# Kernel optimization log

Hardware: AMD Instinct MI355X
Metric: run time of the kernel (lower is better)

## Reference

```python
import jax, jax.numpy as jnp
import numpy as np

EPS = 1e-10      # normalizer eps from the torch module
IN_EPS = 1e-5    # torch InstanceNorm2d default eps
STRIDE = 2
PAD = 1


def _dw_conv_transpose(x, W):
    """Depthwise ConvTranspose2d applied for every output channel at once.

    x: [B, Cin, H, W]
    W: [Cin, Cout, kh, kw]  (W[:, i] is sub_convs[i].weight of shape [Cin, 1, kh, kw])
    returns: [B, Cin, Cout, H', W'] where channel (c, i) = convT of x[:, c] with W[c, i].
    """
    Cin, Cout, kh, kw = W.shape
    # Transposed conv == dilated conv with spatially flipped kernel,
    # lhs_dilation = stride, padding = k - 1 - pad (output_padding = 0).
    rhs = jnp.flip(W, axis=(-2, -1)).reshape(Cin * Cout, 1, kh, kw)
    pad_h = (kh - 1 - PAD, kh - 1 - PAD)
    pad_w = (kw - 1 - PAD, kw - 1 - PAD)
    out = jax.lax.conv_general_dilated(
        x, rhs,
        window_strides=(1, 1),
        padding=(pad_h, pad_w),
        lhs_dilation=(STRIDE, STRIDE),
        dimension_numbers=('NCHW', 'OIHW', 'NCHW'),
        feature_group_count=Cin,
    )  # [B, Cin*Cout, H', W'], group-major: group c -> channels c*Cout:(c+1)*Cout
    B = x.shape[0]
    return out.reshape(B, Cin, Cout, out.shape[2], out.shape[3])


def setup_inputs() -> dict:
    key = jax.random.key(0)
    k1, k2, k3 = jax.random.split(key, 3)
    B, Cin, Cout, H, Wd, K = 2, 64, 64, 48, 48, 4
    x = jax.random.normal(k1, (B, Cin, H, Wd), dtype=jnp.float32)
    # Positive-leaning weights keep the normalizer (convT of ones) away from zero.
    W = 0.05 + 0.1 * jax.random.uniform(k2, (Cin, Cout, K, K), dtype=jnp.float32)
    bias = 0.02 * jax.random.normal(k3, (Cout,), dtype=jnp.float32)
    return {"x": x, "W": W, "bias": bias}


def reference(x, W, bias):
    # numerator: depthwise convT of the input for every (in_ch, out_ch) pair
    num = _dw_conv_transpose(x, W)                       # [B, Cin, Cout, H', W']
    # normalizer: same convT applied to ones (batch-independent -> batch of 1)
    den = _dw_conv_transpose(jnp.ones_like(x[:1]), W) + EPS  # [1, Cin, Cout, H', W']
    out = jnp.sum(num / den, axis=1) + bias[None, :, None, None]  # [B, Cout, H', W']
    # InstanceNorm2d (no affine, biased variance) over spatial dims per (b, c)
    mean = jnp.mean(out, axis=(2, 3), keepdims=True)
    var = jnp.var(out, axis=(2, 3), keepdims=True)
    return (out - mean) / jnp.sqrt(var + IN_EPS)
```

## Files before the change

kernel.cpp:

```cpp
#include <hip/hip_runtime.h>

#define BB    2
#define CIN   64
#define NI    64
#define HIN   48
#define WIN   48
#define HO    96
#define WO    96
#define EPSN  1e-10f
#define IN_EPS 1e-5f
#define IMG   (HO*WO)
#define NIMG  (BB*NI)
#define PH    50
#define PW    52
#define XPN   (BB*CIN*PH*PW)

__global__ __launch_bounds__(256) void pad_kernel(const float* __restrict__ x,
                                                  float* __restrict__ xpad) {
    const int slice = blockIdx.x >> 1, half = blockIdx.x & 1;
    const float* xs = x + (size_t)slice * (HIN * WIN);
    float* xd = xpad + (size_t)slice * (PH * PW) + half * 25 * PW;
    for (int e = threadIdx.x; e < 25 * PW; e += 256) {
        const int rp = e / PW, pc = e - rp * PW;
        const int h = half * 25 + rp - 1, w = pc - 1;
        float v = 0.f;
        if ((unsigned)h < HIN && (unsigned)w < WIN) v = xs[h * WIN + w];
        xd[e] = v;
    }
}

template <int CS>
__global__ __launch_bounds__(256) void conv_kernel(
        const float* __restrict__ xpad, const float* __restrict__ Wt,
        float* __restrict__ part) {
    constexpr int NC = CIN / CS;
    const int bi = blockIdx.x, s = blockIdx.y;
    const int b = bi >> 6, i = bi & 63, c0 = s * NC;
    const int tid = threadIdx.x;
    const int ty = tid >> 4, tx = tid & 15;

    __shared__ __align__(16) float sF[NC * 16];
    __shared__ float sW[NC * 16];
    __shared__ float sR[NC * 16];
    __shared__ float sFix[384];

    for (int e = tid; e < NC * 16; e += 256) {
        const int c = e >> 4, j = e & 15;
        const float* wp = Wt + ((size_t)(c0 + c) * NI + i) * 16;
        sW[e] = wp[j];
        const int py = (j >> 3) & 1, px = (j >> 2) & 1, a = (j >> 1) & 1, bb = j & 1;
        const int kh = py ? (a ? 2 : 0) : (a ? 3 : 1);
        const int kw = px ? (bb ? 2 : 0) : (bb ? 3 : 1);
        const int r0 = py ? 0 : 1, r1 = py ? 2 : 3;
        const int q0 = px ? 0 : 1, q1 = px ? 2 : 3;
        const float den = wp[r0 * 4 + q0] + wp[r0 * 4 + q1]
                        + wp[r1 * 4 + q0] + wp[r1 * 4 + q1];
        sF[e] = wp[kh * 4 + kw] / (den + EPSN);
        const int cy = j >> 2, cx = j & 3;
        const int THn[4] = {1, 2, 2, 1};
        const int THv[4][2] = {{1, 1}, {0, 2}, {1, 3}, {2, 2}};
        float den2 = 0.f;
        for (int aa = 0; aa < THn[cy]; ++aa)
            for (int bb2 = 0; bb2 < THn[cx]; ++bb2)
                den2 += wp[THv[cy][aa] * 4 + THv[cx][bb2]];
        sR[e] = 1.f / (den2 + EPSN);
    }
    __syncthreads();

    float acc[6][6];
#pragma unroll
    for (int r = 0; r < 6; ++r)
#pragma unroll
        for (int j = 0; j < 6; ++j) acc[r][j] = 0.f;

    const float* xb = xpad + ((size_t)b * CIN + c0) * (PH * PW) + (3 * ty) * PW + 3 * tx;

#pragma unroll 2
    for (int c = 0; c < NC; ++c) {
        float g[16];
        const float4* gf = (const float4*)&sF[c * 16];
#pragma unroll
        for (int q = 0; q < 4; ++q) {
            const float4 t = gf[q];
            g[4 * q] = t.x; g[4 * q + 1] = t.y; g[4 * q + 2] = t.z; g[4 * q + 3] = t.w;
        }

        const float* xc = xb + c * (PH * PW);
        float xv[5][5];
#pragma unroll
        for (int rr = 0; rr < 5; ++rr)
#pragma unroll
            for (int cc = 0; cc < 5; ++cc) xv[rr][cc] = xc[rr * PW + cc];

#pragma unroll
        for (int r = 0; r < 6; ++r) {
            const int rhi = (r + 3) >> 1, rlo = rhi - 1, py = r & 1;
#pragma unroll
            for (int j = 0; j < 6; ++j) {
                const int chi = (j + 3) >> 1, clo = chi - 1, px = j & 1;
                const float* gg = &g[py * 8 + px * 4];
                acc[r][j] += xv[rhi][chi] * gg[0] + xv[rhi][clo] * gg[1]
                           + xv[rlo][chi] * gg[2] + xv[rlo][clo] * gg[3];
            }
        }
    }

    const float* xb2 = xpad + ((size_t)b * CIN + c0) * (PH * PW);
    for (int p = tid; p < 380; p += 256) {
        int y, xo;
        if (p < 96)       { y = 0;            xo = p; }
        else if (p < 192) { y = 95;           xo = p - 96; }
        else if (p < 286) { y = p - 192 + 1;  xo = 0; }
        else              { y = p - 286 + 1;  xo = 95; }
        const int hA = (y + 1) >> 1, hB = hA - 1;
        const int khA = (y & 1) ? 0 : 1, khB = khA + 2;
        const int wA = (xo + 1) >> 1, wB = wA - 1;
        const int kwA = (xo & 1) ? 0 : 1, kwB = kwA + 2;
        const int cy = (y == 0) ? 0 : (y == 95) ? 3 : ((y & 1) ? 1 : 2);
        const int cx = (xo == 0) ? 0 : (xo == 95) ? 3 : ((xo & 1) ? 1 : 2);
        const int cls = cy * 4 + cx;
        const int rA = (hA + 1) * PW, rB = (hB + 1) * PW;
        float v = 0.f;
        for (int c = 0; c < NC; ++c) {
            const float* xc = xb2 + c * (PH * PW);
            const float* wc = &sW[c * 16];
            const float num = xc[rA + wA + 1] * wc[khA * 4 + kwA]
                            + xc[rA + wB + 1] * wc[khA * 4 + kwB]
                            + xc[rB + wA + 1] * wc[khB * 4 + kwA]
                            + xc[rB + wB + 1] * wc[khB * 4 + kwB];
            v += num * sR[c * 16 + cls];
        }
        sFix[p] = v;
    }
    __syncthreads();

#pragma unroll
    for (int r = 0; r < 6; ++r)
#pragma unroll
        for (int j = 0; j < 6; ++j) {
            const int y = 6 * ty + r, xo = 6 * tx + j;
            if (y == 0)        acc[r][j] = sFix[xo];
            else if (y == 95)  acc[r][j] = sFix[96 + xo];
            else if (xo == 0)  acc[r][j] = sFix[192 + y - 1];
            else if (xo == 95) acc[r][j] = sFix[286 + y - 1];
        }

    float* pp = part + ((size_t)s * NIMG + bi) * IMG + (6 * ty) * WO + 6 * tx;
#pragma unroll
    for (int r = 0; r < 6; ++r)
#pragma unroll
        for (int jj = 0; jj < 3; ++jj) {
            float2 v;
            v.x = acc[r][2 * jj];
            v.y = acc[r][2 * jj + 1];
            *(float2*)(pp + r * WO + 2 * jj) = v;
        }
}

template <int CS>
__global__ __launch_bounds__(768) void epilogue_kernel(
        const float* __restrict__ part, const float* __restrict__ bias,
        float* __restrict__ out) {
    const int bi = blockIdx.x;
    const int tid = threadIdx.x;
    const float bv = bias[bi & 63];
    const float4* pb = (const float4*)part + (size_t)bi * (IMG / 4);
    const size_t stride4 = (size_t)NIMG * (IMG / 4);

    float4 v[3];
    float s1 = 0.f, s2 = 0.f;
#pragma unroll
    for (int k = 0; k < 3; ++k) {
        const int idx = k * 768 + tid;
        float4 t = pb[idx];
#pragma unroll
        for (int s = 1; s < CS; ++s) {
            const float4 q = pb[s * stride4 + idx];
            t.x += q.x; t.y += q.y; t.z += q.z; t.w += q.w;
        }
        t.x += bv; t.y += bv; t.z += bv; t.w += bv;
        v[k] = t;
        s1 += t.x + t.y + t.z + t.w;
        s2 += t.x * t.x + t.y * t.y + t.z * t.z + t.w * t.w;
    }

    __shared__ float red[24];
    __shared__ float stat[2];
#pragma unroll
    for (int off = 32; off > 0; off >>= 1) {
        s1 += __shfl_down(s1, off, 64);
        s2 += __shfl_down(s2, off, 64);
    }
    const int w = tid >> 6;
    if ((tid & 63) == 0) { red[w] = s1; red[12 + w] = s2; }
    __syncthreads();
    if (tid == 0) {
        float t1 = 0.f, t2 = 0.f;
#pragma unroll
        for (int k = 0; k < 12; ++k) { t1 += red[k]; t2 += red[12 + k]; }
        const float mean = t1 * (1.f / 9216.f);
        const float m2 = t2 * (1.f / 9216.f);
        stat[0] = mean;
        stat[1] = rsqrtf(m2 - mean * mean + IN_EPS);
    }
    __syncthreads();
    const float mean = stat[0], inv = stat[1];

    float4* ob = (float4*)out + (size_t)bi * (IMG / 4);
#pragma unroll
    for (int k = 0; k < 3; ++k) {
        const int idx = k * 768 + tid;
        float4 t = v[k];
        t.x = (t.x - mean) * inv; t.y = (t.y - mean) * inv;
        t.z = (t.z - mean) * inv; t.w = (t.w - mean) * inv;
        ob[idx] = t;
    }
}

extern "C" void kernel_launch(void* const* d_in, const int* in_sizes, int n_in,
                              void* d_out, int out_size, void* d_ws, size_t ws_size,
                              hipStream_t stream) {
    const float* x    = (const float*)d_in[0];
    const float* Wt   = (const float*)d_in[1];
    const float* bias = (const float*)d_in[2];
    float* out = (float*)d_out;
    float* ws  = (float*)d_ws;

    float* xpad = ws;
    pad_kernel<<<BB * CIN * 2, 256, 0, stream>>>(x, xpad);

    const size_t need4 = ((size_t)XPN + (size_t)4 * NIMG * IMG) * 4;
    if (ws_size >= need4) {
        float* part = ws + XPN;
        conv_kernel<4><<<dim3(NIMG, 4), 256, 0, stream>>>(xpad, Wt, part);
        epilogue_kernel<4><<<NIMG, 768, 0, stream>>>(part, bias, out);
    } else {
        conv_kernel<1><<<dim3(NIMG, 1), 256, 0, stream>>>(xpad, Wt, out);
        epilogue_kernel<1><<<NIMG, 768, 0, stream>>>(out, bias, out);
    }
}
```

Measured before the change: 96.68 us.

## Stage input channels in double-buffered LDS and drop separate pad kernel

Removes the padding kernel and its workspace round trip. Each conv block now loads input channel planes straight from global memory into a zero-bordered, double-buffered LDS tile, prefetching the next channel into registers while computing on the current one. The border-fix computation is folded into the same channel loop so it reuses the LDS tile instead of rereading global memory. The cost is a __syncthreads per channel, about 22 KB of extra LDS per block, and a launch bound requesting two blocks per CU.

After: 89.88 us. -7.0%, faster.

```diff
diff --git a/kernel.cpp b/kernel.cpp
--- a/kernel.cpp
+++ b/kernel.cpp
@@ -11,27 +11,13 @@
 #define IN_EPS 1e-5f
 #define IMG   (HO*WO)
 #define NIMG  (BB*NI)
-#define PH    50
-#define PW    52
-#define XPN   (BB*CIN*PH*PW)
-
-__global__ __launch_bounds__(256) void pad_kernel(const float* __restrict__ x,
-                                                  float* __restrict__ xpad) {
-    const int slice = blockIdx.x >> 1, half = blockIdx.x & 1;
-    const float* xs = x + (size_t)slice * (HIN * WIN);
-    float* xd = xpad + (size_t)slice * (PH * PW) + half * 25 * PW;
-    for (int e = threadIdx.x; e < 25 * PW; e += 256) {
-        const int rp = e / PW, pc = e - rp * PW;
-        const int h = half * 25 + rp - 1, w = pc - 1;
-        float v = 0.f;
-        if ((unsigned)h < HIN && (unsigned)w < WIN) v = xs[h * WIN + w];
-        xd[e] = v;
-    }
-}
+#define LPH   50
+#define LPW   56
+#define LPAD  4
 
 template <int CS>
-__global__ __launch_bounds__(256) void conv_kernel(
-        const float* __restrict__ xpad, const float* __restrict__ Wt,
+__global__ __launch_bounds__(256, 2) void conv_kernel(
+        const float* __restrict__ x, const float* __restrict__ Wt,
         float* __restrict__ part) {
     constexpr int NC = CIN / CS;
     const int bi = blockIdx.x, s = blockIdx.y;
@@ -39,11 +25,17 @@
     const int tid = threadIdx.x;
     const int ty = tid >> 4, tx = tid & 15;
 
+    __shared__ __align__(16) float sX[2][LPH * LPW];
     __shared__ __align__(16) float sF[NC * 16];
     __shared__ float sW[NC * 16];
     __shared__ float sR[NC * 16];
     __shared__ float sFix[384];
 
+    {
+        const float4 z = make_float4(0.f, 0.f, 0.f, 0.f);
+        float4* p0 = (float4*)&sX[0][0];
+        for (int e = tid; e < 2 * LPH * LPW / 4; e += 256) p0[e] = z;
+    }
     for (int e = tid; e < NC * 16; e += 256) {
         const int c = e >> 4, j = e & 15;
         const float* wp = Wt + ((size_t)(c0 + c) * NI + i) * 16;
@@ -65,48 +57,22 @@
                 den2 += wp[THv[cy][aa] * 4 + THv[cx][bb2]];
         sR[e] = 1.f / (den2 + EPSN);
     }
-    __syncthreads();
-
-    float acc[6][6];
-#pragma unroll
-    for (int r = 0; r < 6; ++r)
-#pragma unroll
-        for (int j = 0; j < 6; ++j) acc[r][j] = 0.f;
-
-    const float* xb = xpad + ((size_t)b * CIN + c0) * (PH * PW) + (3 * ty) * PW + 3 * tx;
-
-#pragma unroll 2
-    for (int c = 0; c < NC; ++c) {
-        float g[16];
-        const float4* gf = (const float4*)&sF[c * 16];
-#pragma unroll
-        for (int q = 0; q < 4; ++q) {
-            const float4 t = gf[q];
-            g[4 * q] = t.x; g[4 * q + 1] = t.y; g[4 * q + 2] = t.z; g[4 * q + 3] = t.w;
-        }
-
-        const float* xc = xb + c * (PH * PW);
-        float xv[5][5];
-#pragma unroll
-        for (int rr = 0; rr < 5; ++rr)
-#pragma unroll
-            for (int cc = 0; cc < 5; ++cc) xv[rr][cc] = xc[rr * PW + cc];
-
-#pragma unroll
-        for (int r = 0; r < 6; ++r) {
-            const int rhi = (r + 3) >> 1, rlo = rhi - 1, py = r & 1;
-#pragma unroll
-            for (int j = 0; j < 6; ++j) {
-                const int chi = (j + 3) >> 1, clo = chi - 1, px = j & 1;
-                const float* gg = &g[py * 8 + px * 4];
-                acc[r][j] += xv[rhi][chi] * gg[0] + xv[rhi][clo] * gg[1]
-                           + xv[rlo][chi] * gg[2] + xv[rlo][clo] * gg[3];
-            }
-        }
-    }
-
-    const float* xb2 = xpad + ((size_t)b * CIN + c0) * (PH * PW);
-    for (int p = tid; p < 380; p += 256) {
+
+    int ldsOff[3];
+#pragma unroll
+    for (int k = 0; k < 3; ++k) {
+        const int e = tid + 256 * k;
+        const int h = e / 12, w4 = e - 12 * h;
+        ldsOff[k] = (h + 1) * LPW + LPAD + 4 * w4;
+    }
+    const float4* xg = (const float4*)x + (size_t)(b * CIN + c0) * 576;
+
+    int q0A0, q0A1, q0B0, q0B1, w00, w01, w02, w03, cls0;
+    int q1A0, q1A1, q1B0, q1B1, w10, w11, w12, w13, cls1;
+#pragma unroll
+    for (int k = 0; k < 2; ++k) {
+        const int p = tid + 256 * k;
+        if (k == 1 && p >= 380) break;
         int y, xo;
         if (p < 96)       { y = 0;            xo = p; }
         else if (p < 192) { y = 95;           xo = p - 96; }
@@ -118,20 +84,107 @@
         const int kwA = (xo & 1) ? 0 : 1, kwB = kwA + 2;
         const int cy = (y == 0) ? 0 : (y == 95) ? 3 : ((y & 1) ? 1 : 2);
         const int cx = (xo == 0) ? 0 : (xo == 95) ? 3 : ((xo & 1) ? 1 : 2);
-        const int cls = cy * 4 + cx;
-        const int rA = (hA + 1) * PW, rB = (hB + 1) * PW;
-        float v = 0.f;
-        for (int c = 0; c < NC; ++c) {
-            const float* xc = xb2 + c * (PH * PW);
+        const int rA = (hA + 1) * LPW, rB = (hB + 1) * LPW;
+        if (k == 0) {
+            q0A0 = rA + LPAD + wA; q0A1 = rA + LPAD + wB;
+            q0B0 = rB + LPAD + wA; q0B1 = rB + LPAD + wB;
+            w00 = khA * 4 + kwA; w01 = khA * 4 + kwB;
+            w02 = khB * 4 + kwA; w03 = khB * 4 + kwB;
+            cls0 = cy * 4 + cx;
+        } else {
+            q1A0 = rA + LPAD + wA; q1A1 = rA + LPAD + wB;
+            q1B0 = rB + LPAD + wA; q1B1 = rB + LPAD + wB;
+            w10 = khA * 4 + kwA; w11 = khA * 4 + kwB;
+            w12 = khB * 4 + kwA; w13 = khB * 4 + kwB;
+            cls1 = cy * 4 + cx;
+        }
+    }
+
+    __syncthreads();
+
+    {
+        float4 a0 = xg[tid], a1 = xg[tid + 256], a2;
+        if (tid < 64) a2 = xg[tid + 512];
+        float* dst = &sX[0][0];
+        *(float4*)(dst + ldsOff[0]) = a0;
+        *(float4*)(dst + ldsOff[1]) = a1;
+        if (tid < 64) *(float4*)(dst + ldsOff[2]) = a2;
+    }
+    __syncthreads();
+
+    float acc[6][6];
+#pragma unroll
+    for (int r = 0; r < 6; ++r)
+#pragma unroll
+        for (int j = 0; j < 6; ++j) acc[r][j] = 0.f;
+    float fixAcc0 = 0.f, fixAcc1 = 0.f;
+
+    const int patchBase = (3 * ty) * LPW + 3 * tx + (LPAD - 1);
+
+#pragma unroll 2
+    for (int c = 0; c < NC; ++c) {
+        float4 a0, a1, a2;
+        if (c + 1 < NC) {
+            const float4* xn = xg + (size_t)(c + 1) * 576;
+            a0 = xn[tid]; a1 = xn[tid + 256];
+            if (tid < 64) a2 = xn[tid + 512];
+        }
+
+        const float* __restrict__ xs = &sX[c & 1][0];
+
+        float g[16];
+        {
+            const float4* gf = (const float4*)&sF[c * 16];
+#pragma unroll
+            for (int q = 0; q < 4; ++q) {
+                const float4 t = gf[q];
+                g[4 * q] = t.x; g[4 * q + 1] = t.y;
+                g[4 * q + 2] = t.z; g[4 * q + 3] = t.w;
+            }
+        }
+
+        float xv[5][5];
+#pragma unroll
+        for (int rr = 0; rr < 5; ++rr)
+#pragma unroll
+            for (int cc = 0; cc < 5; ++cc)
+                xv[rr][cc] = xs[patchBase + rr * LPW + cc];
+
+#pragma unroll
+        for (int r = 0; r < 6; ++r) {
+            const int rhi = (r + 3) >> 1, rlo = rhi - 1, py = r & 1;
+#pragma unroll
+            for (int j = 0; j < 6; ++j) {
+                const int chi = (j + 3) >> 1, clo = chi - 1, px = j & 1;
+                const float* gg = &g[py * 8 + px * 4];
+                acc[r][j] += xv[rhi][chi] * gg[0] + xv[rhi][clo] * gg[1]
+                           + xv[rlo][chi] * gg[2] + xv[rlo][clo] * gg[3];
+            }
+        }
+
+        {
             const float* wc = &sW[c * 16];
-            const float num = xc[rA + wA + 1] * wc[khA * 4 + kwA]
-                            + xc[rA + wB + 1] * wc[khA * 4 + kwB]
-                            + xc[rB + wA + 1] * wc[khB * 4 + kwA]
-                            + xc[rB + wB + 1] * wc[khB * 4 + kwB];
-            v += num * sR[c * 16 + cls];
-        }
-        sFix[p] = v;
-    }
+            const float num0 = xs[q0A0] * wc[w00] + xs[q0A1] * wc[w01]
+                             + xs[q0B0] * wc[w02] + xs[q0B1] * wc[w03];
+            fixAcc0 += num0 * sR[c * 16 + cls0];
+            if (tid < 124) {
+                const float num1 = xs[q1A0] * wc[w10] + xs[q1A1] * wc[w11]
+                                 + xs[q1B0] * wc[w12] + xs[q1B1] * wc[w13];
+                fixAcc1 += num1 * sR[c * 16 + cls1];
+            }
+        }
+
+        if (c + 1 < NC) {
+            float* dst = &sX[(c + 1) & 1][0];
+            *(float4*)(dst + ldsOff[0]) = a0;
+            *(float4*)(dst + ldsOff[1]) = a1;
+            if (tid < 64) *(float4*)(dst + ldsOff[2]) = a2;
+        }
+        __syncthreads();
+    }
+
+    sFix[tid] = fixAcc0;
+    if (tid < 124) sFix[tid + 256] = fixAcc1;
     __syncthreads();
 
 #pragma unroll
@@ -226,16 +279,12 @@
     float* out = (float*)d_out;
     float* ws  = (float*)d_ws;
 
-    float* xpad = ws;
-    pad_kernel<<<BB * CIN * 2, 256, 0, stream>>>(x, xpad);
-
-    const size_t need4 = ((size_t)XPN + (size_t)4 * NIMG * IMG) * 4;
+    const size_t need4 = (size_t)4 * NIMG * IMG * 4;
     if (ws_size >= need4) {
-        float* part = ws + XPN;
-        conv_kernel<4><<<dim3(NIMG, 4), 256, 0, stream>>>(xpad, Wt, part);
-        epilogue_kernel<4><<<NIMG, 768, 0, stream>>>(part, bias, out);
+        conv_kernel<4><<<dim3(NIMG, 4), 256, 0, stream>>>(x, Wt, ws);
+        epilogue_kernel<4><<<NIMG, 768, 0, stream>>>(ws, bias, out);
     } else {
-        conv_kernel<1><<<dim3(NIMG, 1), 256, 0, stream>>>(xpad, Wt, out);
+        conv_kernel<1><<<dim3(NIMG, 1), 256, 0, stream>>>(x, Wt, out);
         epilogue_kernel<1><<<NIMG, 768, 0, stream>>>(out, bias, out);
     }
 }
```
